# Optimization experiments

Hardware: AMD Instinct MI355X
Metric: run time of the kernel (lower is better)

The kernel has to match this reference:

```python
import jax, jax.numpy as jnp
import numpy as np

N_NODES = 50000
N_EDGES = 600000
EMB_DIM = 128
HIDDEN = 128
BN_EPS = 1e-5


def setup_inputs() -> dict:
    key = jax.random.key(0)
    ks = jax.random.split(key, 8)
    s_in = 1.0 / np.sqrt(EMB_DIM)
    s_h = 1.0 / np.sqrt(HIDDEN)
    return {
        "x_idx": jnp.arange(N_NODES, dtype=jnp.int32),
        "edge_index": jax.random.randint(ks[0], (2, N_EDGES), 0, N_NODES, dtype=jnp.int32),
        "emb_table": jax.random.normal(ks[1], (N_NODES, EMB_DIM), jnp.float32),
        # ClusterGCNConv: lin_out (bias=False) and lin_root (bias=False)
        "W_out": jax.random.uniform(ks[2], (HIDDEN, EMB_DIM), jnp.float32, -s_in, s_in),
        "W_root": jax.random.uniform(ks[3], (HIDDEN, EMB_DIM), jnp.float32, -s_in, s_in),
        "bn0_gamma": jnp.ones((HIDDEN,), jnp.float32),
        "bn0_beta": jnp.zeros((HIDDEN,), jnp.float32),
        # SGConv 1 (K=1, add_self_loops=True, Linear with bias)
        "W_sg1": jax.random.uniform(ks[4], (HIDDEN, HIDDEN), jnp.float32, -s_h, s_h),
        "b_sg1": jnp.zeros((HIDDEN,), jnp.float32),
        "bn1_gamma": jnp.ones((HIDDEN,), jnp.float32),
        "bn1_beta": jnp.zeros((HIDDEN,), jnp.float32),
        # SGConv 2 (final layer)
        "W_sg2": jax.random.uniform(ks[5], (HIDDEN, HIDDEN), jnp.float32, -s_h, s_h),
        "b_sg2": jnp.zeros((HIDDEN,), jnp.float32),
    }


def _cluster_gcn(x, row, col, W_out, W_root, n):
    # PyG ClusterGCNConv (add_self_loops=False, diag_lambda=0, bias=False):
    # out[c] = sum_{(r->c)} (1/deg(c)) * x[r];  return out @ W_out^T + x @ W_root^T
    deg = jax.ops.segment_sum(jnp.ones_like(col, dtype=x.dtype), col, num_segments=n)
    deg_inv = 1.0 / jnp.maximum(deg, 1.0)
    msg = x[row] * deg_inv[col][:, None]                  # [E, D]
    agg = jax.ops.segment_sum(msg, col, num_segments=n)   # [N, D]
    return agg @ W_out.T + x @ W_root.T


def _sg_conv(x, row, col, W, b, n):
    # PyG SGConv K=1 with gcn_norm: A_hat = D^{-1/2}(A+I)D^{-1/2}, then Linear.
    loop = jnp.arange(n, dtype=row.dtype)
    r = jnp.concatenate([row, loop])
    c = jnp.concatenate([col, loop])
    deg = jax.ops.segment_sum(jnp.ones_like(c, dtype=x.dtype), c, num_segments=n)
    dis = jnp.where(deg > 0, jax.lax.rsqrt(jnp.maximum(deg, 1e-12)), 0.0)
    ew = dis[r] * dis[c]                                   # [E+N]
    agg = jax.ops.segment_sum(x[r] * ew[:, None], c, num_segments=n)
    return agg @ W.T + b


def _bn(x, gamma, beta):
    # BatchNorm1d in training mode: batch statistics, biased variance.
    mu = x.mean(axis=0)
    var = ((x - mu) ** 2).mean(axis=0)
    return (x - mu) * jax.lax.rsqrt(var + BN_EPS) * gamma + beta


def reference(x_idx, edge_index, emb_table, W_out, W_root, bn0_gamma, bn0_beta,
              W_sg1, b_sg1, bn1_gamma, bn1_beta, W_sg2, b_sg2):
    n = emb_table.shape[0]
    row, col = edge_index[0], edge_index[1]
    x = emb_table[x_idx]                                   # [N, D]
    # layer 0: ClusterGCNConv -> BN -> ReLU (dropout p=0)
    x = _cluster_gcn(x, row, col, W_out, W_root, n)
    x = jax.nn.relu(_bn(x, bn0_gamma, bn0_beta))
    # layer 1: SGConv -> BN -> ReLU
    x = _sg_conv(x, row, col, W_sg1, b_sg1, n)
    x = jax.nn.relu(_bn(x, bn1_gamma, bn1_beta))
    # final SGConv
    return _sg_conv(x, row, col, W_sg2, b_sg2, n)
```

## Files before the change

kernel.cpp:

```cpp
#include <hip/hip_runtime.h>
#include <stdint.h>

#define NN 50000
#define NE 600000
#define DD 128
#define BN_EPS 1e-5f

typedef __attribute__((ext_vector_type(8))) short short8;
typedef __attribute__((ext_vector_type(4))) float f32x4;

__device__ __forceinline__ float bf2f(uint16_t u) {
    union { uint32_t u; float f; } v; v.u = ((uint32_t)u) << 16; return v.f;
}
__device__ __forceinline__ uint16_t f2bf(float f) {
    union { float f; uint32_t u; } v; v.f = f;
    return (uint16_t)((v.u + 0x7FFFu + ((v.u >> 16) & 1u)) >> 16);
}
__device__ __forceinline__ float lo16(uint32_t v) { return bf2f((uint16_t)(v & 0xFFFFu)); }
__device__ __forceinline__ float hi16(uint32_t v) { return bf2f((uint16_t)(v >> 16)); }

__global__ void k_zero(uint4* __restrict__ p, int n16) {
    int i = blockIdx.x * 256 + threadIdx.x;
    if (i < n16) p[i] = make_uint4(0u, 0u, 0u, 0u);
}

#define EB ((NE + 255) / 256)
#define VB ((NN * 32) / 256)
#define WB 32
__global__ void k_pre(const int* __restrict__ ei, int* __restrict__ cnt,
                      const int* __restrict__ x_idx, const float* __restrict__ emb,
                      uint16_t* __restrict__ xb,
                      const float* __restrict__ Wa, const float* __restrict__ Wb_,
                      const float* __restrict__ Wc, const float* __restrict__ Wd,
                      uint16_t* __restrict__ wb) {
    int b = blockIdx.x;
    if (b < EB) {
        int e = b * 256 + threadIdx.x;
        if (e < NE) atomicAdd(&cnt[ei[NE + e]], 1);
    } else if (b < EB + VB) {
        int idx = (b - EB) * 256 + threadIdx.x;
        int node = idx >> 5, c4 = (idx & 31) << 2;
        int src = x_idx[node];
        float4 v = *(const float4*)(emb + (size_t)src * DD + c4);
        ushort4 o;
        o.x = f2bf(v.x); o.y = f2bf(v.y); o.z = f2bf(v.z); o.w = f2bf(v.w);
        *(ushort4*)(xb + (size_t)node * DD + c4) = o;
    } else {
        int idx = (b - EB - VB) * 256 + threadIdx.x;
        int w = idx >> 11, rem = idx & 2047;
        const float* src = (w == 0) ? Wa : (w == 1) ? Wb_ : (w == 2) ? Wc : Wd;
        float4 v0 = *(const float4*)(src + rem * 8);
        float4 v1 = *(const float4*)(src + rem * 8 + 4);
        uint4 pk;
        pk.x = (uint32_t)f2bf(v0.x) | ((uint32_t)f2bf(v0.y) << 16);
        pk.y = (uint32_t)f2bf(v0.z) | ((uint32_t)f2bf(v0.w) << 16);
        pk.z = (uint32_t)f2bf(v1.x) | ((uint32_t)f2bf(v1.y) << 16);
        pk.w = (uint32_t)f2bf(v1.z) | ((uint32_t)f2bf(v1.w) << 16);
        *(uint4*)(wb + (size_t)w * 16384 + rem * 8) = pk;
    }
}

__global__ void k_alloc(const int* __restrict__ cnt, int* __restrict__ cursor,
                        int* __restrict__ off, int* __restrict__ fillp,
                        float* __restrict__ deginv, float* __restrict__ dis) {
    int i = blockIdx.x * 256 + threadIdx.x;
    int lane = threadIdx.x & 63;
    int deg = (i < NN) ? cnt[i] : 0;
    int v = deg;
    #pragma unroll
    for (int d = 1; d < 64; d <<= 1) {
        int t = __shfl_up(v, d, 64);
        if (lane >= d) v += t;
    }
    int total = __shfl(v, 63, 64);
    int wbase = 0;
    if (lane == 63) wbase = atomicAdd(cursor, total);
    wbase = __shfl(wbase, 63, 64);
    int base = wbase + v - deg;
    if (i < NN) {
        off[i] = base;
        fillp[i] = base;
        deginv[i] = 1.0f / fmaxf((float)deg, 1.0f);
        dis[i] = rsqrtf((float)deg + 1.0f);
    }
}

__global__ void k_fill(const int* __restrict__ ei, int* __restrict__ fillp,
                       int* __restrict__ csr_row) {
    int e = blockIdx.x * 256 + threadIdx.x;
    if (e < NE) {
        int c = ei[NE + e];
        int p = atomicAdd(&fillp[c], 1);
        csr_row[p] = ei[e];
    }
}

template<int MODE>
__global__ __launch_bounds__(256)
void k_agg(const uint16_t* __restrict__ X, const int* __restrict__ off,
           const int* __restrict__ cnt, const int* __restrict__ csr_row,
           const float* __restrict__ deginv, const float* __restrict__ dis,
           uint16_t* __restrict__ aggb) {
    int gw = blockIdx.x * 4 + (threadIdx.x >> 6);
    int lane = threadIdx.x & 63;
    int hl = lane & 31;
    int node = gw * 2 + (lane >> 5);
    if (node >= NN) return;
    float a0 = 0.0f, a1 = 0.0f, a2 = 0.0f, a3 = 0.0f;
    if (MODE == 1) {
        uint2 v = ((const uint2*)(X + (size_t)node * DD))[hl];
        a0 = lo16(v.x); a1 = hi16(v.x); a2 = lo16(v.y); a3 = hi16(v.y);
    }
    int s = off[node], deg = cnt[node];
    int degO = __shfl(deg, lane ^ 32, 64);
    int mdeg = max(deg, degO);
    for (int b = 0; b < mdeg; b += 32) {
        int c32 = min(deg - b, 32);
        int idxv = (hl < c32) ? csr_row[s + b + hl] : 0;
        int steps = min(mdeg - b, 32);
        int i = 0;
        for (; i + 8 <= steps; i += 8) {
            uint2 v[8]; float w[8];
            #pragma unroll
            for (int u = 0; u < 8; ++u) {
                int r = __shfl(idxv, (lane & 32) + i + u, 64);
                w[u] = (b + i + u < deg) ? 1.0f : 0.0f;
                v[u] = ((const uint2*)(X + (size_t)r * DD))[hl];
            }
            #pragma unroll
            for (int u = 0; u < 8; ++u) {
                a0 = fmaf(w[u], lo16(v[u].x), a0);
                a1 = fmaf(w[u], hi16(v[u].x), a1);
                a2 = fmaf(w[u], lo16(v[u].y), a2);
                a3 = fmaf(w[u], hi16(v[u].y), a3);
            }
        }
        if (i + 4 <= steps) {
            uint2 v[4]; float w[4];
            #pragma unroll
            for (int u = 0; u < 4; ++u) {
                int r = __shfl(idxv, (lane & 32) + i + u, 64);
                w[u] = (b + i + u < deg) ? 1.0f : 0.0f;
                v[u] = ((const uint2*)(X + (size_t)r * DD))[hl];
            }
            #pragma unroll
            for (int u = 0; u < 4; ++u) {
                a0 = fmaf(w[u], lo16(v[u].x), a0);
                a1 = fmaf(w[u], hi16(v[u].x), a1);
                a2 = fmaf(w[u], lo16(v[u].y), a2);
                a3 = fmaf(w[u], hi16(v[u].y), a3);
            }
            i += 4;
        }
        for (; i < steps; ++i) {
            int r = __shfl(idxv, (lane & 32) + i, 64);
            float w = (b + i < deg) ? 1.0f : 0.0f;
            uint2 v = ((const uint2*)(X + (size_t)r * DD))[hl];
            a0 = fmaf(w, lo16(v.x), a0);
            a1 = fmaf(w, hi16(v.x), a1);
            a2 = fmaf(w, lo16(v.y), a2);
            a3 = fmaf(w, hi16(v.y), a3);
        }
    }
    float sc = (MODE == 1) ? dis[node] : deginv[node];
    a0 *= sc; a1 *= sc; a2 *= sc; a3 *= sc;
    uint2 o;
    o.x = (uint32_t)f2bf(a0) | ((uint32_t)f2bf(a1) << 16);
    o.y = (uint32_t)f2bf(a2) | ((uint32_t)f2bf(a3) << 16);
    ((uint2*)(aggb + (size_t)node * DD))[hl] = o;
}

template<bool DUAL, bool STATS, bool BIAS, bool STORE_BF16>
__global__ __launch_bounds__(256, 2)
void k_gemm(const uint16_t* __restrict__ A1, const uint16_t* __restrict__ A2,
            const uint16_t* __restrict__ Wb1, const uint16_t* __restrict__ Wb2,
            const float* __restrict__ bias, float* __restrict__ Hf,
            uint16_t* __restrict__ Hb, float* __restrict__ stats) {
    constexpr int NW = DUAL ? 2 : 1;
    __shared__ uint16_t Wlds[NW * 128 * 128];
    const int t = threadIdx.x;
    const int lane = t & 63, wid = t >> 6;
    const int wm = (wid >> 1) * 64, wn = (wid & 1) * 64;
    const int m0 = blockIdx.x * 128;
    #pragma unroll
    for (int w = 0; w < NW; ++w) {
        const uint16_t* Ws = w ? Wb2 : Wb1;
        #pragma unroll
        for (int it = 0; it < 8; ++it) {
            int idx = it * 256 + t;
            int row = idx >> 4, c16 = idx & 15;
            uint4 v = *(const uint4*)(Ws + row * DD + c16 * 8);
            uint32_t boff = (uint32_t)(w * 32768 + row * 256 + ((c16 * 16) ^ ((row & 7) << 4)));
            *(uint4*)((char*)Wlds + boff) = v;
        }
    }
    __syncthreads();
    f32x4 zero = {0.0f, 0.0f, 0.0f, 0.0f};
    f32x4 acc[4][4];
    #pragma unroll
    for (int m = 0; m < 4; ++m)
        #pragma unroll
        for (int n = 0; n < 4; ++n) acc[m][n] = zero;

    #pragma unroll
    for (int ks = 0; ks < NW * 4; ++ks) {
        const uint16_t* A = (DUAL && ks >= 4) ? A2 : A1;
        const int kk = ks & 3;
        const int kb = kk * 64 + ((lane >> 4) << 4);
        short8 a[4], b[4];
        #pragma unroll
        for (int m = 0; m < 4; ++m) {
            int row = m0 + wm + m * 16 + (lane & 15);
            row = min(row, NN - 1);
            a[m] = *(const short8*)(A + (size_t)row * DD + kk * 32 + ((lane >> 4) << 3));
        }
        #pragma unroll
        for (int n = 0; n < 4; ++n) {
            int row = wn + n * 16 + (lane & 15);
            b[n] = *(const short8*)((const char*)Wlds + (ks >= 4 ? 32768 : 0)
                                    + row * 256 + (kb ^ ((row & 7) << 4)));
        }
        #pragma unroll
        for (int m = 0; m < 4; ++m)
            #pragma unroll
            for (int n = 0; n < 4; ++n)
                acc[m][n] = __builtin_amdgcn_mfma_f32_16x16x32_bf16(a[m], b[n], acc[m][n], 0, 0, 0);
    }
    #pragma unroll
    for (int n = 0; n < 4; ++n) {
        int col = wn + n * 16 + (lane & 15);
        float bb = BIAS ? bias[col] : 0.0f;
        float ssum = 0.0f, ssq = 0.0f;
        #pragma unroll
        for (int m = 0; m < 4; ++m) {
            int rbase = m0 + wm + m * 16 + ((lane >> 4) << 2);
            #pragma unroll
            for (int i = 0; i < 4; ++i) {
                int gr = rbase + i;
                if (gr < NN) {
                    float v = acc[m][n][i] + bb;
                    if (STORE_BF16) Hb[(size_t)gr * DD + col] = f2bf(v);
                    else            Hf[(size_t)gr * DD + col] = v;
                    ssum += v; ssq += v * v;
                }
            }
        }
        if (STATS) {
            ssum += __shfl_xor(ssum, 16, 64);
            ssum += __shfl_xor(ssum, 32, 64);
            ssq  += __shfl_xor(ssq, 16, 64);
            ssq  += __shfl_xor(ssq, 32, 64);
            if (lane < 16) {
                atomicAdd(&stats[col], ssum);
                atomicAdd(&stats[DD + col], ssq);
            }
        }
    }
}

__global__ __launch_bounds__(256)
void k_bnrelu(const uint16_t* __restrict__ Hb, const float* __restrict__ st,
              const float* __restrict__ gamma, const float* __restrict__ beta,
              const float* __restrict__ dis, uint16_t* __restrict__ xb) {
    __shared__ float s_sc[128], s_of[128];
    int t = threadIdx.x;
    if (t < 128) {
        const float invn = 1.0f / (float)NN;
        float mean = st[t] * invn;
        float var = st[DD + t] * invn - mean * mean;
        float sc = gamma[t] * rsqrtf(var + BN_EPS);
        s_sc[t] = sc;
        s_of[t] = beta[t] - mean * sc;
    }
    __syncthreads();
    int idx = blockIdx.x * 256 + t;
    int node = idx >> 4, c8 = (idx & 15) << 3;
    if (node >= NN) return;
    float d = dis[node];
    uint4 h = *(const uint4*)(Hb + (size_t)node * DD + c8);
    uint32_t hw[4] = {h.x, h.y, h.z, h.w};
    uint32_t ow[4];
    #pragma unroll
    for (int j = 0; j < 4; ++j) {
        int c = c8 + j * 2;
        float v0 = fmaxf(lo16(hw[j]) * s_sc[c]     + s_of[c],     0.0f) * d;
        float v1 = fmaxf(hi16(hw[j]) * s_sc[c + 1] + s_of[c + 1], 0.0f) * d;
        ow[j] = (uint32_t)f2bf(v0) | ((uint32_t)f2bf(v1) << 16);
    }
    uint4 o = make_uint4(ow[0], ow[1], ow[2], ow[3]);
    *(uint4*)(xb + (size_t)node * DD + c8) = o;
}

extern "C" void kernel_launch(void* const* d_in, const int* in_sizes, int n_in,
                              void* d_out, int out_size, void* d_ws, size_t ws_size,
                              hipStream_t stream) {
    const int* x_idx   = (const int*)d_in[0];
    const int* ei      = (const int*)d_in[1];
    const float* emb   = (const float*)d_in[2];
    const float* W_out = (const float*)d_in[3];
    const float* W_root= (const float*)d_in[4];
    const float* g0    = (const float*)d_in[5];
    const float* be0   = (const float*)d_in[6];
    const float* W1    = (const float*)d_in[7];
    const float* b1    = (const float*)d_in[8];
    const float* g1    = (const float*)d_in[9];
    const float* be1   = (const float*)d_in[10];
    const float* W2    = (const float*)d_in[11];
    const float* b2    = (const float*)d_in[12];
    float* out = (float*)d_out;

    char* ws = (char*)d_ws;
    size_t o = 0;
    auto carve = [&](size_t bytes) -> void* {
        void* p = ws + o;
        o = (o + bytes + 255) & ~(size_t)255;
        return p;
    };
    int* cnt      = (int*)carve((size_t)NN * 4);
    int* cursor   = (int*)carve(4);
    float* st0    = (float*)carve(256 * 4);
    float* st1    = (float*)carve(256 * 4);
    size_t zlen = o;
    int* fillp    = (int*)carve((size_t)NN * 4);
    int* off      = (int*)carve((size_t)NN * 4);
    float* deginv = (float*)carve((size_t)NN * 4);
    float* dis    = (float*)carve((size_t)NN * 4);
    int* csr_row  = (int*)carve((size_t)NE * 4);
    uint16_t* xb  = (uint16_t*)carve((size_t)NN * DD * 2);
    uint16_t* aggb= (uint16_t*)carve((size_t)NN * DD * 2);
    uint16_t* hb  = (uint16_t*)carve((size_t)NN * DD * 2);
    uint16_t* wb  = (uint16_t*)carve((size_t)4 * 16384 * 2);

    const int ZB = (int)((zlen / 16 + 255) / 256);
    const int NB = (NN + 255) / 256;
    const int GB = (NN + 127) / 128;
    const int AB = (NN / 2 + 3) / 4;
    const int BB = (NN * 16 + 255) / 256;

    k_zero<<<ZB, 256, 0, stream>>>((uint4*)ws, (int)(zlen / 16));
    k_pre<<<EB + VB + WB, 256, 0, stream>>>(ei, cnt, x_idx, emb, xb,
                                            W_out, W_root, W1, W2, wb);
    k_alloc<<<NB, 256, 0, stream>>>(cnt, cursor, off, fillp, deginv, dis);
    k_fill<<<EB, 256, 0, stream>>>(ei, fillp, csr_row);

    k_agg<0><<<AB, 256, 0, stream>>>(xb, off, cnt, csr_row, deginv, dis, aggb);
    k_gemm<true, true, false, true><<<GB, 256, 0, stream>>>(
        aggb, xb, wb, wb + 16384, nullptr, nullptr, hb, st0);
    k_bnrelu<<<BB, 256, 0, stream>>>(hb, st0, g0, be0, dis, xb);

    k_agg<1><<<AB, 256, 0, stream>>>(xb, off, cnt, csr_row, deginv, dis, aggb);
    k_gemm<false, true, true, true><<<GB, 256, 0, stream>>>(
        aggb, nullptr, wb + 32768, nullptr, b1, nullptr, hb, st1);
    k_bnrelu<<<BB, 256, 0, stream>>>(hb, st1, g1, be1, dis, xb);

    k_agg<1><<<AB, 256, 0, stream>>>(xb, off, cnt, csr_row, deginv, dis, aggb);
    k_gemm<false, false, true, false><<<GB, 256, 0, stream>>>(
        aggb, nullptr, wb + 49152, nullptr, b2, out, nullptr, nullptr);
}
```

Measured before the change: 249.0 us.

## Drop LDS weight staging in GEMM, use 16-row warp tiles with direct global B loads

The GEMM kernel no longer stages the weight matrix into shared memory. Each warp now computes a 16x128 tile, reading A once and B fragments straight from global memory (L1/L2 cached), with 64 rows per block and a higher occupancy bound. BN statistics atomics are spread over four replicated stat buffers by warp index to reduce contention, and the BN kernel sums the four copies. The trade-off is more global/L2 traffic for B and less A reuse per warp, in exchange for removing the LDS fill, its barrier, and register pressure.

```diff
diff --git a/kernel.cpp b/kernel.cpp
--- a/kernel.cpp
+++ b/kernel.cpp
@@ -171,78 +171,51 @@
 }
 
 template<bool DUAL, bool STATS, bool BIAS, bool STORE_BF16>
-__global__ __launch_bounds__(256, 2)
+__global__ __launch_bounds__(256, 4)
 void k_gemm(const uint16_t* __restrict__ A1, const uint16_t* __restrict__ A2,
             const uint16_t* __restrict__ Wb1, const uint16_t* __restrict__ Wb2,
             const float* __restrict__ bias, float* __restrict__ Hf,
             uint16_t* __restrict__ Hb, float* __restrict__ stats) {
-    constexpr int NW = DUAL ? 2 : 1;
-    __shared__ uint16_t Wlds[NW * 128 * 128];
     const int t = threadIdx.x;
     const int lane = t & 63, wid = t >> 6;
-    const int wm = (wid >> 1) * 64, wn = (wid & 1) * 64;
-    const int m0 = blockIdx.x * 128;
-    #pragma unroll
-    for (int w = 0; w < NW; ++w) {
-        const uint16_t* Ws = w ? Wb2 : Wb1;
+    const int r0 = blockIdx.x * 64 + wid * 16;
+    const int l15 = lane & 15, kgrp = lane >> 4;
+    int arow = min(r0 + l15, NN - 1);
+    const size_t abyte = (size_t)arow * DD + kgrp * 8;
+    const int wbyte = l15 * DD + kgrp * 8;
+    f32x4 acc[8];
+    #pragma unroll
+    for (int n = 0; n < 8; ++n) acc[n] = f32x4{0.0f, 0.0f, 0.0f, 0.0f};
+
+    #pragma unroll
+    for (int ks = 0; ks < (DUAL ? 8 : 4); ++ks) {
+        const uint16_t* A = (DUAL && ks >= 4) ? A2 : A1;
+        const uint16_t* W = (DUAL && ks >= 4) ? Wb2 : Wb1;
+        const int kk = ks & 3;
+        short8 a = *(const short8*)(A + abyte + kk * 32);
+        short8 b[8];
         #pragma unroll
-        for (int it = 0; it < 8; ++it) {
-            int idx = it * 256 + t;
-            int row = idx >> 4, c16 = idx & 15;
-            uint4 v = *(const uint4*)(Ws + row * DD + c16 * 8);
-            uint32_t boff = (uint32_t)(w * 32768 + row * 256 + ((c16 * 16) ^ ((row & 7) << 4)));
-            *(uint4*)((char*)Wlds + boff) = v;
-        }
-    }
-    __syncthreads();
-    f32x4 zero = {0.0f, 0.0f, 0.0f, 0.0f};
-    f32x4 acc[4][4];
-    #pragma unroll
-    for (int m = 0; m < 4; ++m)
+        for (int n = 0; n < 8; ++n)
+            b[n] = *(const short8*)(W + wbyte + n * 16 * DD + kk * 32);
         #pragma unroll
-        for (int n = 0; n < 4; ++n) acc[m][n] = zero;
-
-    #pragma unroll
-    for (int ks = 0; ks < NW * 4; ++ks) {
-        const uint16_t* A = (DUAL && ks >= 4) ? A2 : A1;
-        const int kk = ks & 3;
-        const int kb = kk * 64 + ((lane >> 4) << 4);
-        short8 a[4], b[4];
-        #pragma unroll
-        for (int m = 0; m < 4; ++m) {
-            int row = m0 + wm + m * 16 + (lane & 15);
-            row = min(row, NN - 1);
-            a[m] = *(const short8*)(A + (size_t)row * DD + kk * 32 + ((lane >> 4) << 3));
-        }
-        #pragma unroll
-        for (int n = 0; n < 4; ++n) {
-            int row = wn + n * 16 + (lane & 15);
-            b[n] = *(const short8*)((const char*)Wlds + (ks >= 4 ? 32768 : 0)
-                                    + row * 256 + (kb ^ ((row & 7) << 4)));
-        }
-        #pragma unroll
-        for (int m = 0; m < 4; ++m)
-            #pragma unroll
-            for (int n = 0; n < 4; ++n)
-                acc[m][n] = __builtin_amdgcn_mfma_f32_16x16x32_bf16(a[m], b[n], acc[m][n], 0, 0, 0);
-    }
-    #pragma unroll
-    for (int n = 0; n < 4; ++n) {
-        int col = wn + n * 16 + (lane & 15);
+        for (int n = 0; n < 8; ++n)
+            acc[n] = __builtin_amdgcn_mfma_f32_16x16x32_bf16(a, b[n], acc[n], 0, 0, 0);
+    }
+    float* stc = STATS ? stats + (wid & 3) * 256 : nullptr;
+    #pragma unroll
+    for (int n = 0; n < 8; ++n) {
+        int col = n * 16 + l15;
         float bb = BIAS ? bias[col] : 0.0f;
         float ssum = 0.0f, ssq = 0.0f;
+        int rbase = r0 + kgrp * 4;
         #pragma unroll
-        for (int m = 0; m < 4; ++m) {
-            int rbase = m0 + wm + m * 16 + ((lane >> 4) << 2);
-            #pragma unroll
-            for (int i = 0; i < 4; ++i) {
-                int gr = rbase + i;
-                if (gr < NN) {
-                    float v = acc[m][n][i] + bb;
-                    if (STORE_BF16) Hb[(size_t)gr * DD + col] = f2bf(v);
-                    else            Hf[(size_t)gr * DD + col] = v;
-                    ssum += v; ssq += v * v;
-                }
+        for (int i = 0; i < 4; ++i) {
+            int gr = rbase + i;
+            if (gr < NN) {
+                float v = acc[n][i] + bb;
+                if (STORE_BF16) Hb[(size_t)gr * DD + col] = f2bf(v);
+                else            Hf[(size_t)gr * DD + col] = v;
+                ssum += v; ssq += v * v;
             }
         }
         if (STATS) {
@@ -251,8 +224,8 @@
             ssq  += __shfl_xor(ssq, 16, 64);
             ssq  += __shfl_xor(ssq, 32, 64);
             if (lane < 16) {
-                atomicAdd(&stats[col], ssum);
-                atomicAdd(&stats[DD + col], ssq);
+                atomicAdd(&stc[col], ssum);
+                atomicAdd(&stc[128 + col], ssq);
             }
         }
     }
@@ -266,8 +239,10 @@
     int t = threadIdx.x;
     if (t < 128) {
         const float invn = 1.0f / (float)NN;
-        float mean = st[t] * invn;
-        float var = st[DD + t] * invn - mean * mean;
+        float sum = st[t] + st[256 + t] + st[512 + t] + st[768 + t];
+        float sq  = st[128 + t] + st[384 + t] + st[640 + t] + st[896 + t];
+        float mean = sum * invn;
+        float var = sq * invn - mean * mean;
         float sc = gamma[t] * rsqrtf(var + BN_EPS);
         s_sc[t] = sc;
         s_of[t] = beta[t] - mean * sc;
@@ -318,8 +293,8 @@
     };
     int* cnt      = (int*)carve((size_t)NN * 4);
     int* cursor   = (int*)carve(4);
-    float* st0    = (float*)carve(256 * 4);
-    float* st1    = (float*)carve(256 * 4);
+    float* st0    = (float*)carve(1024 * 4);
+    float* st1    = (float*)carve(1024 * 4);
     size_t zlen = o;
     int* fillp    = (int*)carve((size_t)NN * 4);
     int* off      = (int*)carve((size_t)NN * 4);
@@ -333,7 +308,7 @@
 
     const int ZB = (int)((zlen / 16 + 255) / 256);
     const int NB = (NN + 255) / 256;
-    const int GB = (NN + 127) / 128;
+    const int GB = (NN + 63) / 64;
     const int AB = (NN / 2 + 3) / 4;
     const int BB = (NN * 16 + 255) / 256;
 
```

New measurement: 295.8 us. 1.19x slower.
